# Optimization experiments

Hardware: AMD Instinct MI355X
Metric: run time of the kernel (lower is better)

The kernel has to match this reference:

```python
import jax, jax.numpy as jnp
import numpy as np
from jax import lax

B, CIN, IMG = 32, 3, 128   # batch, image channels, image size
D, K = 256, 512            # codebook dim, codebook size


def _conv(x, w, stride, pad):
    # PyTorch Conv2d (bias=False), NCHW / OIHW
    return lax.conv_general_dilated(x, w, (stride, stride), ((pad, pad), (pad, pad)),
                                    dimension_numbers=('NCHW', 'OIHW', 'NCHW'))


def _deconv(x, w, b):
    # PyTorch ConvTranspose2d(k=4, s=2, p=1): lhs_dilation=2, pad=k-1-p=2, flipped kernel,
    # weight layout (in, out, kh, kw) -> 'IOHW'
    y = lax.conv_general_dilated(x, jnp.flip(w, (2, 3)), (1, 1), ((2, 2), (2, 2)),
                                 lhs_dilation=(2, 2),
                                 dimension_numbers=('NCHW', 'IOHW', 'NCHW'))
    return y + b[None, :, None, None]


def _res(x, w1, w2):
    # Faithful to the source ResidualBlock: relu1 output is DISCARDED (conv1 applied to x)
    out = _conv(x, w1, 1, 1)      # 3x3, pad 1
    out = jax.nn.relu(out)
    out = _conv(out, w2, 1, 0)    # 1x1, pad 0
    return out + x


def setup_inputs() -> dict:
    key = jax.random.key(0)
    ks = jax.random.split(key, 20)
    s = 0.05
    inp = {
        'x': jax.random.uniform(ks[0], (B, CIN, IMG, IMG), jnp.float32),
        # codebook, init uniform(-1/K, 1/K) as in init_weights
        'embed_w': jax.random.uniform(ks[1], (K, D), jnp.float32, -1.0 / K, 1.0 / K),
        # encoder
        'e_w1': jax.random.normal(ks[2], (D, CIN, 4, 4), jnp.float32) * s,
        'e_w2': jax.random.normal(ks[3], (D, D, 4, 4), jnp.float32) * s,
        'e_r1a': jax.random.normal(ks[4], (D, D, 3, 3), jnp.float32) * s,
        'e_r1b': jax.random.normal(ks[5], (D, D, 1, 1), jnp.float32) * s,
        'e_r2a': jax.random.normal(ks[6], (D, D, 3, 3), jnp.float32) * s,
        'e_r2b': jax.random.normal(ks[7], (D, D, 1, 1), jnp.float32) * s,
        # decoder
        'd_r1a': jax.random.normal(ks[8], (D, D, 3, 3), jnp.float32) * s,
        'd_r1b': jax.random.normal(ks[9], (D, D, 1, 1), jnp.float32) * s,
        'd_r2a': jax.random.normal(ks[10], (D, D, 3, 3), jnp.float32) * s,
        'd_r2b': jax.random.normal(ks[11], (D, D, 1, 1), jnp.float32) * s,
        'dt1_w': jax.random.normal(ks[12], (D, D, 4, 4), jnp.float32) * s,  # (in,out,kh,kw)
        'dt1_b': jnp.zeros((D,), jnp.float32),
        'dt2_w': jax.random.normal(ks[13], (D, CIN, 4, 4), jnp.float32) * s,
        'dt2_b': jnp.zeros((CIN,), jnp.float32),
    }
    return inp


def reference(x, embed_w, e_w1, e_w2, e_r1a, e_r1b, e_r2a, e_r2b,
              d_r1a, d_r1b, d_r2a, d_r2b, dt1_w, dt1_b, dt2_w, dt2_b):
    # ---- encoder (BN layers exist but are never called in the source forward) ----
    h = jax.nn.relu(_conv(x, e_w1, 2, 1))          # (B,D,64,64)
    h = jax.nn.relu(_conv(h, e_w2, 2, 1))          # (B,D,32,32)
    h = _res(h, e_r1a, e_r1b)
    z_e = _res(h, e_r2a, e_r2b)                    # (B,D,H,W)

    # ---- vector quantisation ----
    ze = jnp.transpose(z_e, (0, 2, 3, 1))          # (B,H,W,D)
    # squared L2 distances via expansion (same argmin/values as the broadcast diff tensor)
    d2 = (jnp.sum(ze * ze, -1, keepdims=True)      # (B,H,W,1)
          - 2.0 * jnp.einsum('bhwd,kd->bhwk', ze, embed_w)
          + jnp.sum(embed_w * embed_w, -1))        # (B,H,W,K)
    dist = jnp.sqrt(jnp.maximum(d2, 0.0))          # torch.norm(p=2) before min
    idx = jnp.argmin(dist, axis=-1)                # (B,H,W)
    z_q = embed_w[idx]                             # (B,H,W,D) gather

    # losses: source averages over an extra duplicated K axis, identical to mean over B,H,W
    sg = lax.stop_gradient
    loss1 = jnp.mean(jnp.sum((ze - sg(z_q)) ** 2, -1))   # grads -> encoder
    loss2 = jnp.mean(jnp.sum((sg(ze) - z_q) ** 2, -1))   # grads -> codebook

    # ---- decoder (takes z_q; BN layers never called; relu after deconv1 only) ----
    dq = jnp.transpose(z_q, (0, 3, 1, 2))          # (B,D,H,W)
    dq = _res(dq, d_r1a, d_r1b)
    dq = _res(dq, d_r2a, d_r2b)
    dq = jax.nn.relu(_deconv(dq, dt1_w, dt1_b))    # (B,D,64,64)
    recon = jax.nn.sigmoid(_deconv(dq, dt2_w, dt2_b))  # (B,3,128,128)
    return recon, loss1, loss2
```

## Files before the change

kernel.cpp:

```cpp
#include <hip/hip_runtime.h>


typedef __attribute__((ext_vector_type(8))) short bf16x8;
typedef __attribute__((ext_vector_type(4))) float f32x4;
#define MFMA_B16(a, b, c) __builtin_amdgcn_mfma_f32_16x16x32_bf16(a, b, c, 0, 0, 0)

__device__ inline unsigned short f2b(float f) {
    unsigned int u = __float_as_uint(f);
    unsigned int r = u + 0x7fffu + ((u >> 16) & 1u);
    return (unsigned short)(r >> 16);
}
__device__ inline float b2f(unsigned short u) {
    return __uint_as_float(((unsigned int)u) << 16);
}

struct PermfArgs {
    const float* src[10];
    int kw[10];
    int so[10], si[10], sh[10], sw[10];
    int cum[11];
};

__global__ void permf_all_k(PermfArgs a, unsigned short* __restrict__ dst)
{
    int gid = blockIdx.x * 256 + threadIdx.x;
    if (gid >= a.cum[10]) return;
    int seg = 0;
    while (seg < 9 && gid >= a.cum[seg + 1]) ++seg;
    int l = gid - a.cum[seg];
    int q = l & 31;
    int n = (l >> 5) & 255;
    int rest = l >> 13;
    int cch = rest & 7;
    int khkw = rest >> 3;
    int kh = khkw / a.kw[seg], kw = khkw % a.kw[seg];
    int ci = cch * 32 + q;
    dst[gid] = f2b(a.src[seg][n * a.so[seg] + ci * a.si[seg] + kh * a.sh[seg] + kw * a.sw[seg]]);
}

__global__ void misc_prep_k(const float* __restrict__ dt2_w, unsigned short* __restrict__ wg,
                            const float* __restrict__ embed, unsigned short* __restrict__ embF,
                            const float* __restrict__ e_w1, unsigned short* __restrict__ wgc,
                            float* __restrict__ nrm, float* __restrict__ lacc)
{
    int blk = blockIdx.x, tid = threadIdx.x;
    if (blk < 48) {
        int idx = blk * 256 + tid;
        int q = idx & 31;
        int n = (idx >> 5) % 48;
        int cch = idx / (48 * 32);
        int ci = cch * 32 + q;
        int oc = n % 3, khkw = n / 3;
        int kh = khkw >> 2, kw = khkw & 3;
        wg[idx] = f2b(dt2_w[ci * 48 + oc * 16 + kh * 4 + kw]);
    } else if (blk < 560) {
        int idx = (blk - 48) * 256 + tid;
        int q = idx & 31;
        int n = (idx >> 5) & 511;
        int cch = idx >> 14;
        embF[idx] = f2b(embed[n * 256 + cch * 32 + q]);
    } else if (blk < 624) {
        int idx = (blk - 560) * 256 + tid;
        int q = idx & 31;
        int n = (idx >> 5) & 255;
        int kt = idx >> 13;
        int k = kt * 32 + q;
        float v = 0.f;
        if (k < 48) {
            int ci = k >> 4, kh = (k >> 2) & 3, kwv = k & 3;
            v = e_w1[n * 48 + ci * 16 + kh * 4 + kwv];
        }
        wgc[idx] = f2b(v);
    } else if (blk < 752) {
        int row = (blk - 624) * 4 + (tid >> 6);
        int lane = tid & 63;
        float s = 0.f;
        #pragma unroll
        for (int c = 0; c < 256; c += 64) {
            float v = embed[row * 256 + c + lane];
            s += v * v;
        }
        #pragma unroll
        for (int off = 1; off < 64; off <<= 1) s += __shfl_xor(s, off);
        if (lane == 0) nrm[row] = s;
    } else {
        if (tid == 0) lacc[0] = 0.f;
    }
}

__global__ void lossfin_k(const float* __restrict__ lacc, float* __restrict__ out)
{
    if (threadIdx.x == 0) {
        float m = lacc[0] * (1.0f / 32768.0f);
        out[1572864] = m;
        out[1572865] = m;
    }
}

__global__ void __launch_bounds__(256, 4)
conv1m_k(const float* __restrict__ x, const unsigned short* __restrict__ wgc,
         unsigned short* __restrict__ out)
{
    int bh = blockIdx.x;
    int b = bh >> 6, oh = bh & 63;
    int tid = threadIdx.x;
    int lane = tid & 63, wv = tid >> 6;
    int m = lane & 15, quad = lane >> 4;
    __shared__ float xrow[3][4][130];
    __shared__ __align__(16) unsigned short imc[64 * 72];
    for (int s = tid; s < 1560; s += 256) {
        int col = s % 130;
        int t = s / 130;
        int r = t & 3;
        int c = t >> 2;
        int ih = 2 * oh - 1 + r, iw = col - 1;
        float v = 0.f;
        if ((unsigned)ih < 128u && (unsigned)iw < 128u)
            v = x[(((b * 3 + c) << 7) + ih) * 128 + iw];
        xrow[c][r][col] = v;
    }
    __syncthreads();
    for (int s = tid; s < 4096; s += 256) {
        int px = s >> 6, k = s & 63;
        float v = 0.f;
        if (k < 48) {
            int ci = k >> 4, kh = (k >> 2) & 3, kw = k & 3;
            v = xrow[ci][kh][2 * px + kw];
        }
        imc[px * 72 + k] = f2b(v);
    }
    __syncthreads();
    f32x4 acc[16];
    f32x4 z = {0.f, 0.f, 0.f, 0.f};
    #pragma unroll
    for (int i = 0; i < 16; ++i) acc[i] = z;
    bf16x8 a0 = *(const bf16x8*)&imc[((wv << 4) + m) * 72 + (quad << 3)];
    bf16x8 a1 = *(const bf16x8*)&imc[((wv << 4) + m) * 72 + 32 + (quad << 3)];
    #pragma unroll
    for (int nt = 0; nt < 16; ++nt) {
        bf16x8 b0 = *(const bf16x8*)&wgc[(nt * 16 + m) * 32 + (quad << 3)];
        bf16x8 b1 = *(const bf16x8*)&wgc[(256 + nt * 16 + m) * 32 + (quad << 3)];
        acc[nt] = MFMA_B16(a0, b0, acc[nt]);
        acc[nt] = MFMA_B16(a1, b1, acc[nt]);
    }
    #pragma unroll
    for (int nt = 0; nt < 16; ++nt)
        #pragma unroll
        for (int r = 0; r < 4; ++r) {
            int px = (wv << 4) + quad * 4 + r;
            out[(((bh << 6) + px) << 8) + nt * 16 + (lane & 15)] = f2b(fmaxf(acc[nt][r], 0.f));
        }
}

__global__ void __launch_bounds__(256, 3)
mconv2_k(const unsigned short* __restrict__ in, const unsigned short* __restrict__ wf,
         unsigned short* __restrict__ out)
{
    int blk = blockIdx.x;
    int bb = blk >> 4, j = blk & 15;
    int lane = threadIdx.x & 63;
    int n0 = (threadIdx.x >> 6) << 6;
    int m = lane & 15, quad = lane >> 4;
    __shared__ __align__(16) unsigned short win[2 * 66 * 132];
    f32x4 acc[2][2][4];
    f32x4 z = {0.f, 0.f, 0.f, 0.f};
    #pragma unroll
    for (int a = 0; a < 2; ++a)
        #pragma unroll
        for (int i = 0; i < 2; ++i)
            #pragma unroll
            for (int t = 0; t < 4; ++t) acc[a][i][t] = z;

    for (int c0 = 0; c0 < 256; c0 += 128) {
        for (int kh = 0; kh < 4; ++kh) {
            __syncthreads();
            for (int s = threadIdx.x; s < 2 * 66 * 16; s += 256) {
                int c16 = s & 15;
                int t2 = s >> 4;
                int col = t2 % 66;
                int rr = t2 / 66;
                int ih = 4 * j - 1 + kh + 2 * rr, iw = col - 1;
                int4 v = make_int4(0, 0, 0, 0);
                if ((unsigned)ih < 64u && (unsigned)iw < 64u)
                    v = *(const int4*)&in[((((bb << 6) + ih) << 6) + iw) * 256 + c0 + (c16 << 3)];
                int cs = (col >> 1) + (col & 1) * 33;
                *(int4*)&win[(rr * 66 + cs) * 132 + (c16 << 3)] = v;
            }
            __syncthreads();
            #pragma unroll
            for (int kw = 0; kw < 4; ++kw) {
                int csoff = (kw >> 1) + (kw & 1) * 33;
                #pragma unroll
                for (int cch = 0; cch < 4; ++cch) {
                    bf16x8 a00 = *(const bf16x8*)&win[(m + csoff) * 132 + (cch << 5) + (quad << 3)];
                    bf16x8 a01 = *(const bf16x8*)&win[(m + 16 + csoff) * 132 + (cch << 5) + (quad << 3)];
                    bf16x8 a10 = *(const bf16x8*)&win[(66 + m + csoff) * 132 + (cch << 5) + (quad << 3)];
                    bf16x8 a11 = *(const bf16x8*)&win[(66 + m + 16 + csoff) * 132 + (cch << 5) + (quad << 3)];
                    int cg = (c0 >> 5) + cch;
                    int wbase = ((((kh << 2) + kw) * 8 + cg) * 256 + n0 + m) * 32 + (quad << 3);
                    bf16x8 b0 = *(const bf16x8*)&wf[wbase];
                    bf16x8 b1 = *(const bf16x8*)&wf[wbase + 16 * 32];
                    bf16x8 b2 = *(const bf16x8*)&wf[wbase + 32 * 32];
                    bf16x8 b3 = *(const bf16x8*)&wf[wbase + 48 * 32];
                    acc[0][0][0] = MFMA_B16(a00, b0, acc[0][0][0]);
                    acc[0][0][1] = MFMA_B16(a00, b1, acc[0][0][1]);
                    acc[0][0][2] = MFMA_B16(a00, b2, acc[0][0][2]);
                    acc[0][0][3] = MFMA_B16(a00, b3, acc[0][0][3]);
                    acc[0][1][0] = MFMA_B16(a01, b0, acc[0][1][0]);
                    acc[0][1][1] = MFMA_B16(a01, b1, acc[0][1][1]);
                    acc[0][1][2] = MFMA_B16(a01, b2, acc[0][1][2]);
                    acc[0][1][3] = MFMA_B16(a01, b3, acc[0][1][3]);
                    acc[1][0][0] = MFMA_B16(a10, b0, acc[1][0][0]);
                    acc[1][0][1] = MFMA_B16(a10, b1, acc[1][0][1]);
                    acc[1][0][2] = MFMA_B16(a10, b2, acc[1][0][2]);
                    acc[1][0][3] = MFMA_B16(a10, b3, acc[1][0][3]);
                    acc[1][1][0] = MFMA_B16(a11, b0, acc[1][1][0]);
                    acc[1][1][1] = MFMA_B16(a11, b1, acc[1][1][1]);
                    acc[1][1][2] = MFMA_B16(a11, b2, acc[1][1][2]);
                    acc[1][1][3] = MFMA_B16(a11, b3, acc[1][1][3]);
                }
            }
        }
    }
    #pragma unroll
    for (int row = 0; row < 2; ++row) {
        int oh = 2 * j + row;
        #pragma unroll
        for (int mt = 0; mt < 2; ++mt)
            #pragma unroll
            for (int nt = 0; nt < 4; ++nt)
                #pragma unroll
                for (int r = 0; r < 4; ++r) {
                    int px = mt * 16 + quad * 4 + r;
                    int col = n0 + nt * 16 + m;
                    out[((((bb << 5) + oh) << 5) + px) * 256 + col] = f2b(fmaxf(acc[row][mt][nt][r], 0.f));
                }
    }
}

__global__ void __launch_bounds__(256, 3)
mconv3_k(const unsigned short* __restrict__ in, const unsigned short* __restrict__ wf,
         unsigned short* __restrict__ out)
{
    int blk = blockIdx.x;
    int bb = blk >> 4, j = blk & 15;
    int lane = threadIdx.x & 63;
    int n0 = (threadIdx.x >> 6) << 6;
    int m = lane & 15, quad = lane >> 4;
    __shared__ __align__(16) unsigned short win[4 * 34 * 132];
    f32x4 acc[2][2][4];
    f32x4 z = {0.f, 0.f, 0.f, 0.f};
    #pragma unroll
    for (int a = 0; a < 2; ++a)
        #pragma unroll
        for (int i = 0; i < 2; ++i)
            #pragma unroll
            for (int t = 0; t < 4; ++t) acc[a][i][t] = z;

    for (int c0 = 0; c0 < 256; c0 += 128) {
        __syncthreads();
        for (int s = threadIdx.x; s < 4 * 34 * 16; s += 256) {
            int c16 = s & 15;
            int t2 = s >> 4;
            int col = t2 % 34;
            int rr = t2 / 34;
            int ih = 2 * j - 1 + rr, iw = col - 1;
            int4 v = make_int4(0, 0, 0, 0);
            if ((unsigned)ih < 32u && (unsigned)iw < 32u)
                v = *(const int4*)&in[((((bb << 5) + ih) << 5) + iw) * 256 + c0 + (c16 << 3)];
            *(int4*)&win[(rr * 34 + col) * 132 + (c16 << 3)] = v;
        }
        __syncthreads();
        for (int kh = 0; kh < 3; ++kh) {
            #pragma unroll
            for (int kw = 0; kw < 3; ++kw) {
                #pragma unroll
                for (int cch = 0; cch < 4; ++cch) {
                    const unsigned short* ba = &win[(kh * 34 + m + kw) * 132 + (cch << 5) + (quad << 3)];
                    bf16x8 a00 = *(const bf16x8*)ba;
                    bf16x8 a01 = *(const bf16x8*)(ba + 16 * 132);
                    bf16x8 a10 = *(const bf16x8*)(ba + 34 * 132);
                    bf16x8 a11 = *(const bf16x8*)(ba + 50 * 132);
                    int cg = (c0 >> 5) + cch;
                    int wbase = (((kh * 3 + kw) * 8 + cg) * 256 + n0 + m) * 32 + (quad << 3);
                    bf16x8 b0 = *(const bf16x8*)&wf[wbase];
                    bf16x8 b1 = *(const bf16x8*)&wf[wbase + 16 * 32];
                    bf16x8 b2 = *(const bf16x8*)&wf[wbase + 32 * 32];
                    bf16x8 b3 = *(const bf16x8*)&wf[wbase + 48 * 32];
                    acc[0][0][0] = MFMA_B16(a00, b0, acc[0][0][0]);
                    acc[0][0][1] = MFMA_B16(a00, b1, acc[0][0][1]);
                    acc[0][0][2] = MFMA_B16(a00, b2, acc[0][0][2]);
                    acc[0][0][3] = MFMA_B16(a00, b3, acc[0][0][3]);
                    acc[0][1][0] = MFMA_B16(a01, b0, acc[0][1][0]);
                    acc[0][1][1] = MFMA_B16(a01, b1, acc[0][1][1]);
                    acc[0][1][2] = MFMA_B16(a01, b2, acc[0][1][2]);
                    acc[0][1][3] = MFMA_B16(a01, b3, acc[0][1][3]);
                    acc[1][0][0] = MFMA_B16(a10, b0, acc[1][0][0]);
                    acc[1][0][1] = MFMA_B16(a10, b1, acc[1][0][1]);
                    acc[1][0][2] = MFMA_B16(a10, b2, acc[1][0][2]);
                    acc[1][0][3] = MFMA_B16(a10, b3, acc[1][0][3]);
                    acc[1][1][0] = MFMA_B16(a11, b0, acc[1][1][0]);
                    acc[1][1][1] = MFMA_B16(a11, b1, acc[1][1][1]);
                    acc[1][1][2] = MFMA_B16(a11, b2, acc[1][1][2]);
                    acc[1][1][3] = MFMA_B16(a11, b3, acc[1][1][3]);
                }
            }
        }
    }
    #pragma unroll
    for (int row = 0; row < 2; ++row) {
        int oh = 2 * j + row;
        #pragma unroll
        for (int mt = 0; mt < 2; ++mt)
            #pragma unroll
            for (int nt = 0; nt < 4; ++nt)
                #pragma unroll
                for (int r = 0; r < 4; ++r) {
                    int px = mt * 16 + quad * 4 + r;
                    int col = n0 + nt * 16 + m;
                    out[((((bb << 5) + oh) << 5) + px) * 256 + col] = f2b(fmaxf(acc[row][mt][nt][r], 0.f));
                }
    }
}

__global__ void __launch_bounds__(256, 3)
m1x1_k(const unsigned short* __restrict__ in, const unsigned short* __restrict__ wf,
       const unsigned short* __restrict__ res, unsigned short* __restrict__ outb,
       float* __restrict__ outf, int f32out)
{
    int blk = blockIdx.x;
    int lane = threadIdx.x & 63;
    int n0 = (threadIdx.x >> 6) << 6;
    int m = lane & 15, quad = lane >> 4;
    __shared__ __align__(16) unsigned short win[64 * 264];
    f32x4 acc[4][4];
    f32x4 z = {0.f, 0.f, 0.f, 0.f};
    #pragma unroll
    for (int i = 0; i < 4; ++i)
        #pragma unroll
        for (int t = 0; t < 4; ++t) acc[i][t] = z;

    int rowbase = blk << 14;
    for (int s = threadIdx.x; s < 64 * 32; s += 256) {
        int c8 = s & 31, col = s >> 5;
        *(int4*)&win[col * 264 + (c8 << 3)] = *(const int4*)&in[rowbase + (col << 8) + (c8 << 3)];
    }
    __syncthreads();
    #pragma unroll
    for (int cch = 0; cch < 8; ++cch) {
        bf16x8 a0 = *(const bf16x8*)&win[m * 264 + (cch << 5) + (quad << 3)];
        bf16x8 a1 = *(const bf16x8*)&win[(m + 16) * 264 + (cch << 5) + (quad << 3)];
        bf16x8 a2 = *(const bf16x8*)&win[(m + 32) * 264 + (cch << 5) + (quad << 3)];
        bf16x8 a3 = *(const bf16x8*)&win[(m + 48) * 264 + (cch << 5) + (quad << 3)];
        int wbase = (cch * 256 + n0 + m) * 32 + (quad << 3);
        bf16x8 b0 = *(const bf16x8*)&wf[wbase];
        bf16x8 b1 = *(const bf16x8*)&wf[wbase + 16 * 32];
        bf16x8 b2 = *(const bf16x8*)&wf[wbase + 32 * 32];
        bf16x8 b3 = *(const bf16x8*)&wf[wbase + 48 * 32];
        acc[0][0] = MFMA_B16(a0, b0, acc[0][0]);
        acc[0][1] = MFMA_B16(a0, b1, acc[0][1]);
        acc[0][2] = MFMA_B16(a0, b2, acc[0][2]);
        acc[0][3] = MFMA_B16(a0, b3, acc[0][3]);
        acc[1][0] = MFMA_B16(a1, b0, acc[1][0]);
        acc[1][1] = MFMA_B16(a1, b1, acc[1][1]);
        acc[1][2] = MFMA_B16(a1, b2, acc[1][2]);
        acc[1][3] = MFMA_B16(a1, b3, acc[1][3]);
        acc[2][0] = MFMA_B16(a2, b0, acc[2][0]);
        acc[2][1] = MFMA_B16(a2, b1, acc[2][1]);
        acc[2][2] = MFMA_B16(a2, b2, acc[2][2]);
        acc[2][3] = MFMA_B16(a2, b3, acc[2][3]);
        acc[3][0] = MFMA_B16(a3, b0, acc[3][0]);
        acc[3][1] = MFMA_B16(a3, b1, acc[3][1]);
        acc[3][2] = MFMA_B16(a3, b2, acc[3][2]);
        acc[3][3] = MFMA_B16(a3, b3, acc[3][3]);
    }
    #pragma unroll
    for (int mt = 0; mt < 4; ++mt)
        #pragma unroll
        for (int nt = 0; nt < 4; ++nt)
            #pragma unroll
            for (int r = 0; r < 4; ++r) {
                int px = mt * 16 + quad * 4 + r;
                int col = n0 + nt * 16 + m;
                int idx = rowbase + (px << 8) + col;
                float v = acc[mt][nt][r] + b2f(res[idx]);
                outb[idx] = f2b(v);
                if (f32out) outf[idx] = v;
            }
}

__global__ void __launch_bounds__(256, 3)
mdeconv1_k(const unsigned short* __restrict__ in, const unsigned short* __restrict__ wf,
           const float* __restrict__ bias, unsigned short* __restrict__ out)
{
    int blk = blockIdx.x;
    int bb = blk >> 5;
    int rem = blk & 31;
    int pp = rem >> 4;
    int i = rem & 15;
    int oy_a = pp + 4 * i;
    int p = (oy_a + 1) & 1;
    int r0a = (oy_a + 1 - p) >> 1;
    int rbase = r0a - 1;
    int lane = threadIdx.x & 63;
    int n0 = (threadIdx.x >> 6) << 6;
    int m = lane & 15, quad = lane >> 4;
    __shared__ __align__(16) unsigned short win[3 * 34 * 264];

    for (int s = threadIdx.x; s < 3 * 34 * 32; s += 256) {
        int c8 = s & 31;
        int t2 = s >> 5;
        int col = t2 % 34;
        int rr = t2 / 34;
        int ih = rbase + rr, iw = col - 1;
        int4 v = make_int4(0, 0, 0, 0);
        if ((unsigned)ih < 32u && (unsigned)iw < 32u)
            v = *(const int4*)&in[((((bb << 5) + ih) << 5) + iw) * 256 + (c8 << 3)];
        *(int4*)&win[(rr * 34 + col) * 264 + (c8 << 3)] = v;
    }
    __syncthreads();

    for (int par = 0; par < 2; ++par) {
        f32x4 acc[2][2][4];
        f32x4 z = {0.f, 0.f, 0.f, 0.f};
        #pragma unroll
        for (int a = 0; a < 2; ++a)
            #pragma unroll
            for (int i2 = 0; i2 < 2; ++i2)
                #pragma unroll
                for (int t = 0; t < 4; ++t) acc[a][i2][t] = z;

        #pragma unroll
        for (int t = 0; t < 2; ++t) {
            int kh = p + 2 * t;
            #pragma unroll
            for (int u = 0; u < 2; ++u) {
                int kw = (1 - par) + 2 * u;
                int ixoff = par - u + 1;
                #pragma unroll
                for (int cch = 0; cch < 8; ++cch) {
                    const unsigned short* baA = &win[((1 - t) * 34 + m + ixoff) * 264 + (cch << 5) + (quad << 3)];
                    const unsigned short* baB = baA + 34 * 264;
                    bf16x8 a00 = *(const bf16x8*)baA;
                    bf16x8 a01 = *(const bf16x8*)(baA + 16 * 264);
                    bf16x8 a10 = *(const bf16x8*)baB;
                    bf16x8 a11 = *(const bf16x8*)(baB + 16 * 264);
                    int wbase = ((((kh << 2) + kw) * 8 + cch) * 256 + n0 + m) * 32 + (quad << 3);
                    bf16x8 b0 = *(const bf16x8*)&wf[wbase];
                    bf16x8 b1 = *(const bf16x8*)&wf[wbase + 16 * 32];
                    bf16x8 b2 = *(const bf16x8*)&wf[wbase + 32 * 32];
                    bf16x8 b3 = *(const bf16x8*)&wf[wbase + 48 * 32];
                    acc[0][0][0] = MFMA_B16(a00, b0, acc[0][0][0]);
                    acc[0][0][1] = MFMA_B16(a00, b1, acc[0][0][1]);
                    acc[0][0][2] = MFMA_B16(a00, b2, acc[0][0][2]);
                    acc[0][0][3] = MFMA_B16(a00, b3, acc[0][0][3]);
                    acc[0][1][0] = MFMA_B16(a01, b0, acc[0][1][0]);
                    acc[0][1][1] = MFMA_B16(a01, b1, acc[0][1][1]);
                    acc[0][1][2] = MFMA_B16(a01, b2, acc[0][1][2]);
                    acc[0][1][3] = MFMA_B16(a01, b3, acc[0][1][3]);
                    acc[1][0][0] = MFMA_B16(a10, b0, acc[1][0][0]);
                    acc[1][0][1] = MFMA_B16(a10, b1, acc[1][0][1]);
                    acc[1][0][2] = MFMA_B16(a10, b2, acc[1][0][2]);
                    acc[1][0][3] = MFMA_B16(a10, b3, acc[1][0][3]);
                    acc[1][1][0] = MFMA_B16(a11, b0, acc[1][1][0]);
                    acc[1][1][1] = MFMA_B16(a11, b1, acc[1][1][1]);
                    acc[1][1][2] = MFMA_B16(a11, b2, acc[1][1][2]);
                    acc[1][1][3] = MFMA_B16(a11, b3, acc[1][1][3]);
                }
            }
        }
        #pragma unroll
        for (int row = 0; row < 2; ++row) {
            int oy = oy_a + 2 * row;
            #pragma unroll
            for (int mt = 0; mt < 2; ++mt)
                #pragma unroll
                for (int nt = 0; nt < 4; ++nt) {
                    int col = n0 + nt * 16 + m;
                    float bs = bias[col];
                    #pragma unroll
                    for (int r = 0; r < 4; ++r) {
                        int ox = 2 * (mt * 16 + quad * 4 + r) + par;
                        float v = fmaxf(acc[row][mt][nt][r] + bs, 0.f);
                        out[((((bb << 6) + oy) << 6) + ox) * 256 + col] = f2b(v);
                    }
                }
        }
    }
}

__global__ void __launch_bounds__(256, 2)
vqm_k(const unsigned short* __restrict__ zeb, const float* __restrict__ zef,
      const unsigned short* __restrict__ embF, const float* __restrict__ embed,
      const float* __restrict__ nrm, unsigned short* __restrict__ zq,
      float* __restrict__ lacc)
{
    int bh = blockIdx.x;
    int tid = threadIdx.x;
    int lane = tid & 63;
    int wv = tid >> 6;
    int m = lane & 15, quad = lane >> 4;
    __shared__ __align__(16) unsigned short win[32 * 264];
    __shared__ float bvv[4][32];
    __shared__ int   bii[4][32];
    __shared__ int   bidx[32];
    int rowbase = bh << 13;
    for (int s = tid; s < 32 * 32; s += 256) {
        int c8 = s & 31, px = s >> 5;
        *(int4*)&win[px * 264 + (c8 << 3)] = *(const int4*)&zeb[rowbase + (px << 8) + (c8 << 3)];
    }
    __syncthreads();

    f32x4 acc[2][8];
    f32x4 z = {0.f, 0.f, 0.f, 0.f};
    #pragma unroll
    for (int i = 0; i < 2; ++i)
        #pragma unroll
        for (int j = 0; j < 8; ++j) acc[i][j] = z;

    #pragma unroll
    for (int cch = 0; cch < 8; ++cch) {
        bf16x8 a0 = *(const bf16x8*)&win[m * 264 + (cch << 5) + (quad << 3)];
        bf16x8 a1 = *(const bf16x8*)&win[(m + 16) * 264 + (cch << 5) + (quad << 3)];
        #pragma unroll
        for (int nt = 0; nt < 8; ++nt) {
            bf16x8 b = *(const bf16x8*)&embF[((cch << 9) + (wv << 7) + (nt << 4) + m) * 32 + (quad << 3)];
            acc[0][nt] = MFMA_B16(a0, b, acc[0][nt]);
            acc[1][nt] = MFMA_B16(a1, b, acc[1][nt]);
        }
    }

    float nv[8];
    #pragma unroll
    for (int nt = 0; nt < 8; ++nt) nv[nt] = nrm[(wv << 7) + (nt << 4) + m];

    #pragma unroll
    for (int mt = 0; mt < 2; ++mt)
        #pragma unroll
        for (int r = 0; r < 4; ++r) {
            float bv = 1e30f;
            int bi = 0x7fffffff;
            #pragma unroll
            for (int nt = 0; nt < 8; ++nt) {
                float d = nv[nt] - 2.f * acc[mt][nt][r];
                int n = (wv << 7) + (nt << 4) + m;
                if (d < bv || (d == bv && n < bi)) { bv = d; bi = n; }
            }
            #pragma unroll
            for (int off = 1; off < 16; off <<= 1) {
                float ov = __shfl_xor(bv, off);
                int oi = __shfl_xor(bi, off);
                if (ov < bv || (ov == bv && oi < bi)) { bv = ov; bi = oi; }
            }
            if (m == 0) {
                int px = mt * 16 + quad * 4 + r;
                bvv[wv][px] = bv;
                bii[wv][px] = bi;
            }
        }
    __syncthreads();
    if (tid < 32) {
        float bv = bvv[0][tid];
        int bi = bii[0][tid];
        #pragma unroll
        for (int w2 = 1; w2 < 4; ++w2) {
            float ov = bvv[w2][tid];
            int oi = bii[w2][tid];
            if (ov < bv || (ov == bv && oi < bi)) { bv = ov; bi = oi; }
        }
        bidx[tid] = bi;
    }
    __syncthreads();

    float lsum = 0.f;
    #pragma unroll
    for (int j = 0; j < 8; ++j) {
        int px = (wv << 3) + j;
        int bi = bidx[px];
        int pix = (bh << 5) + px;
        const float4 e = *(const float4*)&embed[bi * 256 + (lane << 2)];
        const float4 zv = *(const float4*)&zef[(pix << 8) + (lane << 2)];
        ushort4 eq;
        eq.x = f2b(e.x); eq.y = f2b(e.y); eq.z = f2b(e.z); eq.w = f2b(e.w);
        *(ushort4*)&zq[(pix << 8) + (lane << 2)] = eq;
        float dx = zv.x - e.x, dy = zv.y - e.y, dz = zv.z - e.z, dw = zv.w - e.w;
        lsum += dx * dx + dy * dy + dz * dz + dw * dw;
    }
    #pragma unroll
    for (int off = 1; off < 64; off <<= 1) lsum += __shfl_xor(lsum, off);
    if (lane == 0) atomicAdd(lacc, lsum);
}

__global__ void __launch_bounds__(256, 4)
mdec2a_k(const unsigned short* __restrict__ in, const unsigned short* __restrict__ wg,
         float* __restrict__ Y)
{
    int tid = threadIdx.x;
    int lane = tid & 63;
    int wv = tid >> 6;
    int m = lane & 15, quad = lane >> 4;
    __shared__ __align__(16) unsigned short win[64 * 264];
    int pxbase = blockIdx.x << 6;
    for (int s = tid; s < 64 * 32; s += 256) {
        int c8 = s & 31, px = s >> 5;
        *(int4*)&win[px * 264 + (c8 << 3)] = *(const int4*)&in[((pxbase + px) << 8) + (c8 << 3)];
    }
    __syncthreads();
    f32x4 acc[3];
    f32x4 z = {0.f, 0.f, 0.f, 0.f};
    acc[0] = z; acc[1] = z; acc[2] = z;
    #pragma unroll
    for (int cch = 0; cch < 8; ++cch) {
        bf16x8 a = *(const bf16x8*)&win[((wv << 4) + m) * 264 + (cch << 5) + (quad << 3)];
        #pragma unroll
        for (int nt = 0; nt < 3; ++nt) {
            bf16x8 b = *(const bf16x8*)&wg[(cch * 48 + nt * 16 + m) * 32 + (quad << 3)];
            acc[nt] = MFMA_B16(a, b, acc[nt]);
        }
    }
    #pragma unroll
    for (int nt = 0; nt < 3; ++nt)
        #pragma unroll
        for (int r = 0; r < 4; ++r) {
            int px = pxbase + (wv << 4) + quad * 4 + r;
            Y[px * 48 + nt * 16 + m] = acc[nt][r];
        }
}

__global__ void dec2b_k(const float* __restrict__ Y, const float* __restrict__ bias,
                        float* __restrict__ out)
{
    int idx = blockIdx.x * 256 + threadIdx.x;
    int b = idx >> 14;
    int rem = idx & 16383;
    int oy = rem >> 7;
    int ox = rem & 127;
    int p = (oy + 1) & 1;
    int q = (ox + 1) & 1;
    float acc0 = bias[0], acc1 = bias[1], acc2 = bias[2];
    #pragma unroll
    for (int t = 0; t < 2; ++t) {
        int kh = p + 2 * t;
        int ih = (oy + 1 - kh) >> 1;
        if ((unsigned)ih >= 64u) continue;
        #pragma unroll
        for (int u = 0; u < 2; ++u) {
            int kw = q + 2 * u;
            int iw = (ox + 1 - kw) >> 1;
            if ((unsigned)iw >= 64u) continue;
            int base = ((((b << 6) + ih) << 6) + iw) * 48 + ((kh << 2) + kw) * 3;
            acc0 += Y[base];
            acc1 += Y[base + 1];
            acc2 += Y[base + 2];
        }
    }
    int obase = (b * 3 << 14) + (oy << 7) + ox;
    out[obase]           = 1.f / (1.f + expf(-acc0));
    out[obase + 16384]   = 1.f / (1.f + expf(-acc1));
    out[obase + 32768]   = 1.f / (1.f + expf(-acc2));
}

extern "C" void kernel_launch(void* const* d_in, const int* in_sizes, int n_in,
                              void* d_out, int out_size, void* d_ws, size_t ws_size,
                              hipStream_t stream)
{
    (void)in_sizes; (void)n_in; (void)out_size; (void)ws_size;
    const float* x      = (const float*)d_in[0];
    const float* embed  = (const float*)d_in[1];
    const float* e_w1   = (const float*)d_in[2];
    const float* e_w2   = (const float*)d_in[3];
    const float* e_r1a  = (const float*)d_in[4];
    const float* e_r1b  = (const float*)d_in[5];
    const float* e_r2a  = (const float*)d_in[6];
    const float* e_r2b  = (const float*)d_in[7];
    const float* d_r1a  = (const float*)d_in[8];
    const float* d_r1b  = (const float*)d_in[9];
    const float* d_r2a  = (const float*)d_in[10];
    const float* d_r2b  = (const float*)d_in[11];
    const float* dt1_w  = (const float*)d_in[12];
    const float* dt1_b  = (const float*)d_in[13];
    const float* dt2_w  = (const float*)d_in[14];
    const float* dt2_b  = (const float*)d_in[15];
    float* outp = (float*)d_out;

    char* base = (char*)d_ws;
    size_t off = 0;
    auto alloc = [&](size_t bytes) { char* p = base + off; off += (bytes + 255) & ~size_t(255); return p; };
    unsigned short* A0b = (unsigned short*)alloc(67108864);
    float*          A1f = (float*)alloc(33554432);
    unsigned short* L0  = (unsigned short*)alloc(16777216);
    unsigned short* L1  = (unsigned short*)alloc(16777216);
    unsigned short* L2  = (unsigned short*)alloc(16777216);
    unsigned short* Wf  = (unsigned short*)alloc(9437184);
    unsigned short* Wg  = (unsigned short*)alloc(24576);
    unsigned short* EmbF = (unsigned short*)alloc(262144);
    unsigned short* WgC = (unsigned short*)alloc(32768);
    float* Nrm  = (float*)alloc(2048);
    float* Lacc = (float*)alloc(64);
    float* Y = A1f;

    unsigned short* Wf_ew2  = Wf;
    unsigned short* Wf_er1a = Wf + 1048576;
    unsigned short* Wf_er1b = Wf + 1638400;
    unsigned short* Wf_er2a = Wf + 1703936;
    unsigned short* Wf_er2b = Wf + 2293760;
    unsigned short* Wf_dr1a = Wf + 2359296;
    unsigned short* Wf_dr1b = Wf + 2949120;
    unsigned short* Wf_dr2a = Wf + 3014656;
    unsigned short* Wf_dr2b = Wf + 3604480;
    unsigned short* Wf_dt1  = Wf + 3670016;

    PermfArgs pa;
    const float* srcs[10] = {e_w2, e_r1a, e_r1b, e_r2a, e_r2b, d_r1a, d_r1b, d_r2a, d_r2b, dt1_w};
    int kws[10] = {4, 3, 1, 3, 1, 3, 1, 3, 1, 4};
    int sos[10] = {4096, 2304, 256, 2304, 256, 2304, 256, 2304, 256, 16};
    int sis[10] = {16, 9, 1, 9, 1, 9, 1, 9, 1, 4096};
    int shs[10] = {4, 3, 0, 3, 0, 3, 0, 3, 0, 4};
    int sws[10] = {1, 1, 0, 1, 0, 1, 0, 1, 0, 1};
    int cums[11] = {0, 1048576, 1638400, 1703936, 2293760, 2359296,
                    2949120, 3014656, 3604480, 3670016, 4718592};
    for (int k = 0; k < 10; ++k) {
        pa.src[k] = srcs[k]; pa.kw[k] = kws[k]; pa.so[k] = sos[k];
        pa.si[k] = sis[k]; pa.sh[k] = shs[k]; pa.sw[k] = sws[k];
        pa.cum[k] = cums[k];
    }
    pa.cum[10] = cums[10];

    permf_all_k<<<18432, 256, 0, stream>>>(pa, Wf);
    misc_prep_k<<<753, 256, 0, stream>>>(dt2_w, Wg, embed, EmbF, e_w1, WgC, Nrm, Lacc);

    conv1m_k<<<32 * 64, 256, 0, stream>>>(x, WgC, A0b);
    mconv2_k<<<32 * 16, 256, 0, stream>>>(A0b, Wf_ew2, L1);
    mconv3_k<<<32 * 16, 256, 0, stream>>>(L1, Wf_er1a, L2);
    m1x1_k<<<32 * 16, 256, 0, stream>>>(L2, Wf_er1b, L1, L0, nullptr, 0);
    mconv3_k<<<32 * 16, 256, 0, stream>>>(L0, Wf_er2a, L2);
    m1x1_k<<<32 * 16, 256, 0, stream>>>(L2, Wf_er2b, L0, L1, A1f, 1);

    vqm_k<<<32 * 32, 256, 0, stream>>>(L1, A1f, EmbF, embed, Nrm, L1, Lacc);

    mconv3_k<<<32 * 16, 256, 0, stream>>>(L1, Wf_dr1a, L2);
    m1x1_k<<<32 * 16, 256, 0, stream>>>(L2, Wf_dr1b, L1, L0, nullptr, 0);
    mconv3_k<<<32 * 16, 256, 0, stream>>>(L0, Wf_dr2a, L2);
    m1x1_k<<<32 * 16, 256, 0, stream>>>(L2, Wf_dr2b, L0, L1, nullptr, 0);
    mdeconv1_k<<<32 * 32, 256, 0, stream>>>(L1, Wf_dt1, dt1_b, A0b);
    mdec2a_k<<<2048, 256, 0, stream>>>(A0b, Wg, Y);
    dec2b_k<<<2048, 256, 0, stream>>>(Y, dt2_b, outp);
    lossfin_k<<<1, 64, 0, stream>>>(Lacc, outp);
}
```

Measured before the change: 848.0 us.

## Retile deconv1 to four output rows per block with channel-chunked LDS window

The first transposed-conv kernel now gives each block one column parity and four output rows instead of both parities and two rows. The input window is staged in two 128-channel chunks of 5 rows, which keeps LDS use moderate while each weight fragment loaded from global memory feeds twice as many MFMAs. The cost is more accumulator registers, so launch bounds drop from 3 to 2 waves-per-SIMD, plus an extra sync round per chunk and some halo rows loaded by more than one block.

```diff
diff --git a/kernel.cpp b/kernel.cpp
--- a/kernel.cpp
+++ b/kernel.cpp
@@ -389,46 +389,48 @@
             }
 }
 
-__global__ void __launch_bounds__(256, 3)
+__global__ void __launch_bounds__(256, 2)
 mdeconv1_k(const unsigned short* __restrict__ in, const unsigned short* __restrict__ wf,
            const float* __restrict__ bias, unsigned short* __restrict__ out)
 {
     int blk = blockIdx.x;
-    int bb = blk >> 5;
+    int bb  = blk >> 5;
     int rem = blk & 31;
-    int pp = rem >> 4;
-    int i = rem & 15;
-    int oy_a = pp + 4 * i;
+    int par = rem >> 4;
+    int pp  = (rem >> 3) & 1;
+    int i   = rem & 7;
+    int oy_a = pp + 8 * i;
     int p = (oy_a + 1) & 1;
     int r0a = (oy_a + 1 - p) >> 1;
     int rbase = r0a - 1;
     int lane = threadIdx.x & 63;
     int n0 = (threadIdx.x >> 6) << 6;
     int m = lane & 15, quad = lane >> 4;
-    __shared__ __align__(16) unsigned short win[3 * 34 * 264];
-
-    for (int s = threadIdx.x; s < 3 * 34 * 32; s += 256) {
-        int c8 = s & 31;
-        int t2 = s >> 5;
-        int col = t2 % 34;
-        int rr = t2 / 34;
-        int ih = rbase + rr, iw = col - 1;
-        int4 v = make_int4(0, 0, 0, 0);
-        if ((unsigned)ih < 32u && (unsigned)iw < 32u)
-            v = *(const int4*)&in[((((bb << 5) + ih) << 5) + iw) * 256 + (c8 << 3)];
-        *(int4*)&win[(rr * 34 + col) * 264 + (c8 << 3)] = v;
-    }
-    __syncthreads();
-
-    for (int par = 0; par < 2; ++par) {
-        f32x4 acc[2][2][4];
-        f32x4 z = {0.f, 0.f, 0.f, 0.f};
-        #pragma unroll
-        for (int a = 0; a < 2; ++a)
-            #pragma unroll
-            for (int i2 = 0; i2 < 2; ++i2)
-                #pragma unroll
-                for (int t = 0; t < 4; ++t) acc[a][i2][t] = z;
+    __shared__ __align__(16) unsigned short win[5 * 34 * 136];
+
+    f32x4 acc[4][2][4];
+    f32x4 z = {0.f, 0.f, 0.f, 0.f};
+    #pragma unroll
+    for (int r = 0; r < 4; ++r)
+        #pragma unroll
+        for (int i2 = 0; i2 < 2; ++i2)
+            #pragma unroll
+            for (int t = 0; t < 4; ++t) acc[r][i2][t] = z;
+
+    for (int c0 = 0; c0 < 256; c0 += 128) {
+        __syncthreads();
+        for (int s = threadIdx.x; s < 5 * 34 * 16; s += 256) {
+            int c16 = s & 15;
+            int t2 = s >> 4;
+            int col = t2 % 34;
+            int rr = t2 / 34;
+            int ih = rbase + rr, iw = col - 1;
+            int4 v = make_int4(0, 0, 0, 0);
+            if ((unsigned)ih < 32u && (unsigned)iw < 32u)
+                v = *(const int4*)&in[((((bb << 5) + ih) << 5) + iw) * 256 + c0 + (c16 << 3)];
+            *(int4*)&win[(rr * 34 + col) * 136 + (c16 << 3)] = v;
+        }
+        __syncthreads();
 
         #pragma unroll
         for (int t = 0; t < 2; ++t) {
@@ -438,54 +440,53 @@
                 int kw = (1 - par) + 2 * u;
                 int ixoff = par - u + 1;
                 #pragma unroll
-                for (int cch = 0; cch < 8; ++cch) {
-                    const unsigned short* baA = &win[((1 - t) * 34 + m + ixoff) * 264 + (cch << 5) + (quad << 3)];
-                    const unsigned short* baB = baA + 34 * 264;
-                    bf16x8 a00 = *(const bf16x8*)baA;
-                    bf16x8 a01 = *(const bf16x8*)(baA + 16 * 264);
-                    bf16x8 a10 = *(const bf16x8*)baB;
-                    bf16x8 a11 = *(const bf16x8*)(baB + 16 * 264);
-                    int wbase = ((((kh << 2) + kw) * 8 + cch) * 256 + n0 + m) * 32 + (quad << 3);
+                for (int cch = 0; cch < 4; ++cch) {
+                    bf16x8 a[4][2];
+                    #pragma unroll
+                    for (int r = 0; r < 4; ++r) {
+                        const unsigned short* ba =
+                            &win[((1 - t + r) * 34 + m + ixoff) * 136 + (cch << 5) + (quad << 3)];
+                        a[r][0] = *(const bf16x8*)ba;
+                        a[r][1] = *(const bf16x8*)(ba + 16 * 136);
+                    }
+                    int cgl = (c0 >> 5) + cch;
+                    int wbase = ((((kh << 2) + kw) * 8 + cgl) * 256 + n0 + m) * 32 + (quad << 3);
                     bf16x8 b0 = *(const bf16x8*)&wf[wbase];
                     bf16x8 b1 = *(const bf16x8*)&wf[wbase + 16 * 32];
                     bf16x8 b2 = *(const bf16x8*)&wf[wbase + 32 * 32];
                     bf16x8 b3 = *(const bf16x8*)&wf[wbase + 48 * 32];
-                    acc[0][0][0] = MFMA_B16(a00, b0, acc[0][0][0]);
-                    acc[0][0][1] = MFMA_B16(a00, b1, acc[0][0][1]);
-                    acc[0][0][2] = MFMA_B16(a00, b2, acc[0][0][2]);
-                    acc[0][0][3] = MFMA_B16(a00, b3, acc[0][0][3]);
-                    acc[0][1][0] = MFMA_B16(a01, b0, acc[0][1][0]);
-                    acc[0][1][1] = MFMA_B16(a01, b1, acc[0][1][1]);
-                    acc[0][1][2] = MFMA_B16(a01, b2, acc[0][1][2]);
-                    acc[0][1][3] = MFMA_B16(a01, b3, acc[0][1][3]);
-                    acc[1][0][0] = MFMA_B16(a10, b0, acc[1][0][0]);
-                    acc[1][0][1] = MFMA_B16(a10, b1, acc[1][0][1]);
-                    acc[1][0][2] = MFMA_B16(a10, b2, acc[1][0][2]);
-                    acc[1][0][3] = MFMA_B16(a10, b3, acc[1][0][3]);
-                    acc[1][1][0] = MFMA_B16(a11, b0, acc[1][1][0]);
-                    acc[1][1][1] = MFMA_B16(a11, b1, acc[1][1][1]);
-                    acc[1][1][2] = MFMA_B16(a11, b2, acc[1][1][2]);
-                    acc[1][1][3] = MFMA_B16(a11, b3, acc[1][1][3]);
-                }
-            }
-        }
-        #pragma unroll
-        for (int row = 0; row < 2; ++row) {
-            int oy = oy_a + 2 * row;
-            #pragma unroll
-            for (int mt = 0; mt < 2; ++mt)
-                #pragma unroll
-                for (int nt = 0; nt < 4; ++nt) {
-                    int col = n0 + nt * 16 + m;
-                    float bs = bias[col];
                     #pragma unroll
                     for (int r = 0; r < 4; ++r) {
-                        int ox = 2 * (mt * 16 + quad * 4 + r) + par;
-                        float v = fmaxf(acc[row][mt][nt][r] + bs, 0.f);
-                        out[((((bb << 6) + oy) << 6) + ox) * 256 + col] = f2b(v);
+                        acc[r][0][0] = MFMA_B16(a[r][0], b0, acc[r][0][0]);
+                        acc[r][0][1] = MFMA_B16(a[r][0], b1, acc[r][0][1]);
+                        acc[r][0][2] = MFMA_B16(a[r][0], b2, acc[r][0][2]);
+                        acc[r][0][3] = MFMA_B16(a[r][0], b3, acc[r][0][3]);
+                        acc[r][1][0] = MFMA_B16(a[r][1], b0, acc[r][1][0]);
+                        acc[r][1][1] = MFMA_B16(a[r][1], b1, acc[r][1][1]);
+                        acc[r][1][2] = MFMA_B16(a[r][1], b2, acc[r][1][2]);
+                        acc[r][1][3] = MFMA_B16(a[r][1], b3, acc[r][1][3]);
                     }
                 }
-        }
+            }
+        }
+    }
+
+    #pragma unroll
+    for (int r = 0; r < 4; ++r) {
+        int oy = oy_a + 2 * r;
+        #pragma unroll
+        for (int mt = 0; mt < 2; ++mt)
+            #pragma unroll
+            for (int nt = 0; nt < 4; ++nt) {
+                int col = n0 + nt * 16 + m;
+                float bs = bias[col];
+                #pragma unroll
+                for (int rr = 0; rr < 4; ++rr) {
+                    int ox = 2 * (mt * 16 + quad * 4 + rr) + par;
+                    float v = fmaxf(acc[r][mt][nt][rr] + bs, 0.f);
+                    out[((((bb << 6) + oy) << 6) + ox) * 256 + col] = f2b(v);
+                }
+            }
     }
 }
 
```

Result: slower. 884.8 us (+4.3%).
